# Kernel tuning notes

Measured on AMD Instinct MI355X. Metric: run time of the kernel, lower is better.

The kernel has to match this reference:

```python
import jax, jax.numpy as jnp
import numpy as np

EMB = 1024
NHEAD = 16
DILATIONS = (1, 4, 8, 16)
KSIZE = 7
ROT_DIM = 32  # RotaryEmbedding(dim=32): only first 32 channels of each head rotated


def neighbor_idx(T, k, d):
    # NATTEN-style 1D dilated neighborhood: window of k positions on the
    # dilation lattice (same residue class mod d), centered and clamped at borders.
    i = jnp.arange(T)
    r = i % d                      # residue class
    p = i // d                     # position within class
    Lr = (T - r + d - 1) // d      # class length
    s = jnp.clip(p - k // 2, 0, Lr - k)
    j = jnp.arange(k)
    return r[:, None] + (s[:, None] + j[None, :]) * d  # [T, k] int indices


def rope(x, rot_dim=ROT_DIM):
    # lucidrains RotaryEmbedding.rotate_queries_or_keys: interleaved pairs,
    # applied over seq dim (-2), only first rot_dim channels.
    T = x.shape[-2]
    inv = 1.0 / (10000.0 ** (jnp.arange(0, rot_dim, 2, dtype=jnp.float32) / rot_dim))
    freqs = jnp.arange(T, dtype=jnp.float32)[:, None] * inv[None, :]  # [T, rot_dim//2]
    freqs = jnp.repeat(freqs, 2, axis=-1)                             # [T, rot_dim]
    cos, sin = jnp.cos(freqs), jnp.sin(freqs)
    xr, xp = x[..., :rot_dim], x[..., rot_dim:]
    x1, x2 = xr[..., 0::2], xr[..., 1::2]
    rot = jnp.stack([-x2, x1], axis=-1).reshape(xr.shape)
    return jnp.concatenate([xr * cos + rot * sin, xp], axis=-1)


def setup_inputs() -> dict:
    key = jax.random.key(0)
    ks = jax.random.split(key, 5)
    B, T, C = 4, 8192, EMB
    s = 0.02
    return {
        "x": jax.random.normal(ks[0], (B, T, C), jnp.float32),
        "wq": jax.random.normal(ks[1], (C, C), jnp.float32) * s,
        "bq": jnp.zeros((C,), jnp.float32),
        "wk": jax.random.normal(ks[2], (C, C), jnp.float32) * s,
        "bk": jnp.zeros((C,), jnp.float32),
        "wv": jax.random.normal(ks[3], (C, C), jnp.float32) * s,
        "bv": jnp.zeros((C,), jnp.float32),
        "wp": jax.random.normal(ks[4], (C, C), jnp.float32) * s,
        "bp": jnp.zeros((C,), jnp.float32),
    }


def reference(x, wq, bq, wk, bk, wv, bv, wp, bp):
    B, T, C = x.shape
    hs = C // NHEAD

    def heads(w, b):  # torch Linear: x @ W^T + b, then [B, nh, T, hs]
        return (x @ w.T + b).reshape(B, T, NHEAD, hs).transpose(0, 2, 1, 3)

    q, k, v = heads(wq, bq), heads(wk, bk), heads(wv, bv)
    present = jnp.stack([k, v])  # pre-rotary kv cache, as in original

    q, k, v = rope(q), rope(k), rope(v)  # original also rotates v

    gsz = NHEAD // len(DILATIONS)
    outs = []
    for gi, d in enumerate(DILATIONS):
        sl = slice(gi * gsz, (gi + 1) * gsz)
        idx = neighbor_idx(T, KSIZE, d)           # [T, K]
        kk = k[:, sl][:, :, idx]                   # [B, g, T, K, hs]
        vv = v[:, sl][:, :, idx]                   # [B, g, T, K, hs]
        scores = jnp.einsum('bgtd,bgtkd->bgtk', q[:, sl], kk)  # no 1/sqrt(hs), as na1d_qk
        attn = jax.nn.softmax(scores, axis=-1)
        outs.append(jnp.einsum('bgtk,bgtkd->bgtd', attn, vv))
    y = jnp.concatenate(outs, axis=1)              # [B, nh, T, hs]
    y = y.transpose(0, 2, 1, 3).reshape(B, T, C)
    y = y @ wp.T + bp
    return (y, present)
```

## Files before the change

### kernel.cpp

```cpp
#include <hip/hip_runtime.h>

typedef unsigned short ushortT;
typedef unsigned int uint32;
typedef __attribute__((ext_vector_type(8))) short short8;
typedef __attribute__((ext_vector_type(4))) float f32x4;

__device__ __forceinline__ ushortT f2bf(float f) {
    uint32 u = __float_as_uint(f);
    uint32 r = (u + 0x7fffu + ((u >> 16) & 1u)) >> 16;
    return (ushortT)r;
}
__device__ __forceinline__ float bf2f(uint32 v) {
    return __uint_as_float(v << 16);
}

__device__ __forceinline__ void unpack8(uint4 v, float* f) {
    f[0] = bf2f(v.x & 0xffffu); f[1] = bf2f(v.x >> 16);
    f[2] = bf2f(v.y & 0xffffu); f[3] = bf2f(v.y >> 16);
    f[4] = bf2f(v.z & 0xffffu); f[5] = bf2f(v.z >> 16);
    f[6] = bf2f(v.w & 0xffffu); f[7] = bf2f(v.w >> 16);
}

typedef __attribute__((address_space(1))) const void gvoid;
typedef __attribute__((address_space(3))) void lvoid;
__device__ __forceinline__ void gld16(const ushortT* g, ushortT* l) {
    __builtin_amdgcn_global_load_lds((gvoid*)g, (lvoid*)l, 16, 0, 0);
}

__global__ __launch_bounds__(256) void f32_to_bf16_kernel(
    const float* __restrict__ src, ushortT* __restrict__ dst, int n4)
{
    int i = blockIdx.x * 256 + threadIdx.x;
    if (i < n4) {
        float4 v = reinterpret_cast<const float4*>(src)[i];
        ushort4 o;
        o.x = f2bf(v.x); o.y = f2bf(v.y); o.z = f2bf(v.z); o.w = f2bf(v.w);
        reinterpret_cast<ushort4*>(dst)[i] = o;
    }
}

__global__ __launch_bounds__(256) void wconv_kernel(
    const float* __restrict__ s0, const float* __restrict__ s1,
    const float* __restrict__ s2, const float* __restrict__ s3,
    ushortT* __restrict__ dst)
{
    int i = blockIdx.x * 256 + threadIdx.x;
    const int wsel = i >> 18;
    const int off  = i & 262143;
    const float* s = (wsel == 0) ? s0 : (wsel == 1 ? s1 : (wsel == 2 ? s2 : s3));
    float4 v = reinterpret_cast<const float4*>(s)[off];
    ushort4 o;
    o.x = f2bf(v.x); o.y = f2bf(v.y); o.z = f2bf(v.z); o.w = f2bf(v.w);
    reinterpret_cast<ushort4*>(dst)[i] = o;
}

__global__ __launch_bounds__(256) void pack_bias_kernel(
    const float* __restrict__ bq, const float* __restrict__ bk,
    const float* __restrict__ bv, float* __restrict__ out)
{
    int i = blockIdx.x * 256 + threadIdx.x;
    float v = (i < 1024) ? bq[i] : (i < 2048 ? bk[i - 1024] : bv[i - 2048]);
    out[i] = v;
}

__global__ __launch_bounds__(256) void rope_table_kernel(float2* __restrict__ tab)
{
    int idx = blockIdx.x * 256 + threadIdx.x;
    int t = idx >> 4;
    int i = idx & 15;
    float inv = powf(10000.0f, -(float)i / 16.0f);
    float ang = (float)t * inv;
    tab[idx] = make_float2(cosf(ang), sinf(ang));
}


__device__ __forceinline__ short8 ldsfrag(const ushortT* region, int row, int g) {
    int e = (row << 5) + (g << 3);
    e ^= ((row >> 1) & 3) << 3;
    return *reinterpret_cast<const short8*>(region + e);
}

#define MC_ ((size_t)33554432)

template<int MODE>
__global__ __launch_bounds__(256, 3) void gemm128_kernel(
    const ushortT* __restrict__ A,
    const ushortT* __restrict__ Wall,
    const float*   __restrict__ biasAll,
    const float2*  __restrict__ tab,
    ushortT*       __restrict__ CbAll,
    float*         __restrict__ CfAll,
    int M, int N, int K)
{
    __shared__ ushortT lds[16384];
    const int tid  = threadIdx.x;
    const int lane = tid & 63;
    const int wv   = tid >> 6;
    const int wm   = wv >> 1;
    const int wn   = wv & 1;
    const int g    = lane >> 4;
    const int rsel = lane & 15;

    const int bidAll = blockIdx.x;
    const int proj   = (MODE == 3) ? (bidAll >> 11) : 0;
    const int bid    = (MODE == 3) ? (bidAll & 2047) : bidAll;

    const ushortT* W    = Wall + (size_t)proj * 1024 * K;
    const float*   bias = biasAll + proj * 1024;

    const int xi  = bid & 7;
    const int j   = bid >> 3;
    const int tn  = j & 7;
    const int tm  = xi * 32 + (j >> 3);
    const int m0  = tm * 128, n0 = tn * 128;

    const int crow = tid >> 2;
    const int ccol = ((tid & 3) ^ ((tid >> 3) & 3)) * 8;
    const ushortT* gA0 = A + (size_t)(m0 + crow) * K + ccol;
    const ushortT* gA1 = gA0 + (size_t)64 * K;
    const ushortT* gB0 = W + (size_t)(n0 + crow) * K + ccol;
    const ushortT* gB1 = gB0 + (size_t)64 * K;

    const int dst0 = wv * 512;
    const int dst1 = 2048 + wv * 512;

    #define STAGE(buf, t) { \
        ushortT* base_ = lds + (buf) * 8192; \
        gld16(gA0 + (t) * 32, base_ + dst0); \
        gld16(gA1 + (t) * 32, base_ + dst1); \
        gld16(gB0 + (t) * 32, base_ + 4096 + dst0); \
        gld16(gB1 + (t) * 32, base_ + 4096 + dst1); \
    }

    f32x4 acc[4][4] = {};
    const int NT = K >> 5;
    int cur = 0;

    STAGE(0, 0);

    #pragma unroll 1
    for (int t = 0; t < NT; ++t) {
        __syncthreads();
        if (t + 1 < NT) STAGE(cur ^ 1, t + 1);

        const ushortT* ra = lds + cur * 8192;
        const ushortT* rb = ra + 4096;
        short8 Af[4], Bf[4];
        #pragma unroll
        for (int fm = 0; fm < 4; ++fm) Af[fm] = ldsfrag(ra, wm * 64 + fm * 16 + rsel, g);
        #pragma unroll
        for (int fn = 0; fn < 4; ++fn) Bf[fn] = ldsfrag(rb, wn * 64 + fn * 16 + rsel, g);
        #pragma unroll
        for (int fm = 0; fm < 4; ++fm)
            #pragma unroll
            for (int fn = 0; fn < 4; ++fn)
                acc[fm][fn] = __builtin_amdgcn_mfma_f32_16x16x32_bf16(Af[fm], Bf[fn], acc[fm][fn], 0, 0, 0);
        cur ^= 1;
    }
    #undef STAGE

    #pragma unroll
    for (int fn = 0; fn < 4; ++fn) {
        const int colb = n0 + wn * 64 + fn * 16 + rsel;
        const int d    = colb & 63;
        const float bv = bias[colb];
        #pragma unroll
        for (int fm = 0; fm < 4; ++fm) {
            const int rowbase = m0 + wm * 64 + fm * 16 + g * 4;
            #pragma unroll
            for (int e = 0; e < 4; ++e) {
                const int row = rowbase + e;
                const float val = acc[fm][fn][e] + bv;
                if (MODE == 2) {
                    CfAll[(size_t)row * N + colb] = val;
                } else {
                    if (proj != 0) {
                        const int b = row >> 13, t = row & 8191;
                        const int h = colb >> 6;
                        CfAll[(size_t)(proj - 1) * MC_ +
                              (((size_t)b * 16 + h) * 8192 + t) * 64 + d] = val;
                    }
                    const float pv = __shfl_xor(val, 1, 64);
                    float ov = val;
                    if (d < 32) {
                        const int t = row & 8191;
                        const float2 cs = tab[t * 16 + (d >> 1)];
                        ov = (d & 1) ? fmaf(val, cs.x,  pv * cs.y)
                                     : fmaf(val, cs.x, -pv * cs.y);
                    }
                    CbAll[(size_t)proj * MC_ + (size_t)row * 1024 + colb] = f2bf(ov);
                }
            }
        }
    }
}

__global__ __launch_bounds__(256) void natt_kernel(
    const ushortT* __restrict__ Q,
    const ushortT* __restrict__ Kl,
    const ushortT* __restrict__ Vl,
    ushortT*       __restrict__ O)
{
    const int T = 8192;
    const int tid  = threadIdx.x;
    const int lane = tid & 63;
    const int tloc = lane >> 3;
    const int c    = lane & 7;

    const int wq   = (blockIdx.x * 256 + tid) >> 6;
    const int qidx = wq * 8 + tloc;
    const int t = qidx & (T - 1);
    const int h = (qidx >> 13) & 15;
    const int b = qidx >> 17;

    const int shifts[4] = {0, 2, 3, 4};
    const int sh = shifts[h >> 2];
    const int dd = 1 << sh;

    const int r  = t & (dd - 1);
    const int p  = t >> sh;
    const int Lr = ((T - 1 - r) >> sh) + 1;
    int s = p - 3;
    const int smax = Lr - 7;
    s = s < 0 ? 0 : (s > smax ? smax : s);
    const int tbase = r + (s << sh);

    const size_t qoff = ((size_t)(b * T + t)) * 1024 + h * 64 + c * 8;
    float qf[8];
    unpack8(*reinterpret_cast<const uint4*>(Q + qoff), qf);

    const size_t cbase = ((size_t)b * T) * 1024 + h * 64 + c * 8;

    float sc[7];
    #pragma unroll
    for (int j = 0; j < 7; ++j) {
        const int tj = tbase + (j << sh);
        float kf[8];
        unpack8(*reinterpret_cast<const uint4*>(Kl + cbase + (size_t)tj * 1024), kf);
        float pp = 0.f;
        #pragma unroll
        for (int i = 0; i < 8; ++i) pp = fmaf(qf[i], kf[i], pp);
        pp += __shfl_xor(pp, 1, 64);
        pp += __shfl_xor(pp, 2, 64);
        pp += __shfl_xor(pp, 4, 64);
        sc[j] = pp;
    }

    float mx = sc[0];
    #pragma unroll
    for (int j = 1; j < 7; ++j) mx = fmaxf(mx, sc[j]);
    float den = 0.f;
    #pragma unroll
    for (int j = 0; j < 7; ++j) { sc[j] = __expf(sc[j] - mx); den += sc[j]; }
    const float inv = 1.0f / den;

    float out[8] = {};
    #pragma unroll
    for (int j = 0; j < 7; ++j) {
        const int tj = tbase + (j << sh);
        float vf[8];
        unpack8(*reinterpret_cast<const uint4*>(Vl + cbase + (size_t)tj * 1024), vf);
        #pragma unroll
        for (int i = 0; i < 8; ++i) out[i] = fmaf(sc[j], vf[i], out[i]);
    }

    short8 ov;
    #pragma unroll
    for (int i = 0; i < 8; ++i) ov[i] = (short)f2bf(out[i] * inv);
    *reinterpret_cast<short8*>(const_cast<ushortT*>(O + qoff)) = ov;
}

extern "C" void kernel_launch(void* const* d_in, const int* in_sizes, int n_in,
                              void* d_out, int out_size, void* d_ws, size_t ws_size,
                              hipStream_t stream)
{
    const float* x  = (const float*)d_in[0];
    const float* wq = (const float*)d_in[1];
    const float* bq = (const float*)d_in[2];
    const float* wk = (const float*)d_in[3];
    const float* bk = (const float*)d_in[4];
    const float* wv = (const float*)d_in[5];
    const float* bv = (const float*)d_in[6];
    const float* wp = (const float*)d_in[7];
    const float* bp = (const float*)d_in[8];

    const int B = 4, T = 8192, C = 1024;
    const int M = B * T;
    const size_t MC = (size_t)M * C;

    char* ws = (char*)d_ws;
    ushortT* xb    = (ushortT*)ws;
    ushortT* wallb = (ushortT*)(ws + (size_t)64 * 1024 * 1024);
    ushortT* wpb   = wallb + (size_t)3 * C * C;
    ushortT* qlin  = (ushortT*)(ws + (size_t)72 * 1024 * 1024);
    ushortT* klin  = qlin + MC;
    ushortT* vlin  = klin + MC;
    float2*  tab   = (float2*)(ws + (size_t)264 * 1024 * 1024);
    float*   bqkv  = (float*)(ws + (size_t)266 * 1024 * 1024);

    float* y     = (float*)d_out;
    float* presK = y + MC;

    rope_table_kernel<<<512, 256, 0, stream>>>(tab);
    pack_bias_kernel<<<12, 256, 0, stream>>>(bq, bk, bv, bqkv);

    f32_to_bf16_kernel<<<(int)(MC / 4 / 256), 256, 0, stream>>>(x, xb, (int)(MC / 4));
    wconv_kernel<<<4 * (C * C / 4) / 256, 256, 0, stream>>>(wq, wk, wv, wp, wallb);

    gemm128_kernel<3><<<6144, 256, 0, stream>>>(
        xb, wallb, bqkv, tab, qlin, presK, M, C, C);

    natt_kernel<<<(B * 16 * T) / 32, 256, 0, stream>>>(qlin, klin, vlin, xb);

    gemm128_kernel<2><<<2048, 256, 0, stream>>>(
        xb, wpb, bp, tab, nullptr, y, M, C, C);
}
```

Measured before the change: 587.3 us.

## Fuse Q/K/V projections into one GEMM sharing the A tile

The QKV projection kernel now computes all three projections in each block, using a 128x64 tile per projection. Each staged A tile therefore feeds three B tiles instead of being reloaded once per projection, which cuts A-side global and LDS traffic. The trade-off is a larger accumulator set (96 floats per lane) and more shared memory, so the launch bound drops to 2 blocks per CU and occupancy may fall. The output projection becomes its own specialised kernel with launch bound 4.

Result: slower. 716.1 us (+21.9%).

```diff
diff --git a/kernel.cpp b/kernel.cpp
--- a/kernel.cpp
+++ b/kernel.cpp
@@ -73,7 +73,6 @@
     tab[idx] = make_float2(cosf(ang), sinf(ang));
 }
 
-
 __device__ __forceinline__ short8 ldsfrag(const ushortT* region, int row, int g) {
     int e = (row << 5) + (g << 3);
     e ^= ((row >> 1) & 3) << 3;
@@ -82,17 +81,16 @@
 
 #define MC_ ((size_t)33554432)
 
-template<int MODE>
-__global__ __launch_bounds__(256, 3) void gemm128_kernel(
+__global__ __launch_bounds__(256, 2) void gemm_qkv_kernel(
     const ushortT* __restrict__ A,
     const ushortT* __restrict__ Wall,
     const float*   __restrict__ biasAll,
     const float2*  __restrict__ tab,
     ushortT*       __restrict__ CbAll,
     float*         __restrict__ CfAll,
-    int M, int N, int K)
-{
-    __shared__ ushortT lds[16384];
+    int M, int K)
+{
+    __shared__ ushortT lds[2 * 10240];
     const int tid  = threadIdx.x;
     const int lane = tid & 63;
     const int wv   = tid >> 6;
@@ -101,38 +99,35 @@
     const int g    = lane >> 4;
     const int rsel = lane & 15;
 
-    const int bidAll = blockIdx.x;
-    const int proj   = (MODE == 3) ? (bidAll >> 11) : 0;
-    const int bid    = (MODE == 3) ? (bidAll & 2047) : bidAll;
-
-    const ushortT* W    = Wall + (size_t)proj * 1024 * K;
-    const float*   bias = biasAll + proj * 1024;
-
+    const int bid = blockIdx.x;
     const int xi  = bid & 7;
     const int j   = bid >> 3;
-    const int tn  = j & 7;
-    const int tm  = xi * 32 + (j >> 3);
-    const int m0  = tm * 128, n0 = tn * 128;
+    const int tn  = j & 15;
+    const int tm  = xi * 32 + (j >> 4);
+    const int m0  = tm * 128, n0 = tn * 64;
 
     const int crow = tid >> 2;
     const int ccol = ((tid & 3) ^ ((tid >> 3) & 3)) * 8;
     const ushortT* gA0 = A + (size_t)(m0 + crow) * K + ccol;
     const ushortT* gA1 = gA0 + (size_t)64 * K;
-    const ushortT* gB0 = W + (size_t)(n0 + crow) * K + ccol;
-    const ushortT* gB1 = gB0 + (size_t)64 * K;
-
-    const int dst0 = wv * 512;
-    const int dst1 = 2048 + wv * 512;
+    const ushortT* gBq = Wall + (size_t)(n0 + crow) * K + ccol;
+    const ushortT* gBk = gBq + (size_t)1024 * K;
+    const ushortT* gBv = gBq + (size_t)2048 * K;
+
+    const int dA0 = wv * 512;
+    const int dA1 = 2048 + wv * 512;
+    const int dB  = wv * 512;
 
     #define STAGE(buf, t) { \
-        ushortT* base_ = lds + (buf) * 8192; \
-        gld16(gA0 + (t) * 32, base_ + dst0); \
-        gld16(gA1 + (t) * 32, base_ + dst1); \
-        gld16(gB0 + (t) * 32, base_ + 4096 + dst0); \
-        gld16(gB1 + (t) * 32, base_ + 4096 + dst1); \
-    }
-
-    f32x4 acc[4][4] = {};
+        ushortT* b_ = lds + (buf) * 10240; \
+        gld16(gA0 + (t) * 32, b_ + dA0); \
+        gld16(gA1 + (t) * 32, b_ + dA1); \
+        gld16(gBq + (t) * 32, b_ + 4096 + dB); \
+        gld16(gBk + (t) * 32, b_ + 6144 + dB); \
+        gld16(gBv + (t) * 32, b_ + 8192 + dB); \
+    }
+
+    f32x4 acc[3][4][2] = {};
     const int NT = K >> 5;
     int cur = 0;
 
@@ -143,41 +138,47 @@
         __syncthreads();
         if (t + 1 < NT) STAGE(cur ^ 1, t + 1);
 
-        const ushortT* ra = lds + cur * 8192;
-        const ushortT* rb = ra + 4096;
-        short8 Af[4], Bf[4];
-        #pragma unroll
-        for (int fm = 0; fm < 4; ++fm) Af[fm] = ldsfrag(ra, wm * 64 + fm * 16 + rsel, g);
-        #pragma unroll
-        for (int fn = 0; fn < 4; ++fn) Bf[fn] = ldsfrag(rb, wn * 64 + fn * 16 + rsel, g);
+        const ushortT* bb = lds + cur * 10240;
+        short8 Af[4], Bf[3][2];
         #pragma unroll
         for (int fm = 0; fm < 4; ++fm)
+            Af[fm] = ldsfrag(bb, wm * 64 + fm * 16 + rsel, g);
+        #pragma unroll
+        for (int p = 0; p < 3; ++p)
             #pragma unroll
-            for (int fn = 0; fn < 4; ++fn)
-                acc[fm][fn] = __builtin_amdgcn_mfma_f32_16x16x32_bf16(Af[fm], Bf[fn], acc[fm][fn], 0, 0, 0);
+            for (int fn = 0; fn < 2; ++fn)
+                Bf[p][fn] = ldsfrag(bb + 4096 + p * 2048, wn * 32 + fn * 16 + rsel, g);
+
+        #pragma unroll
+        for (int p = 0; p < 3; ++p)
+            #pragma unroll
+            for (int fm = 0; fm < 4; ++fm)
+                #pragma unroll
+                for (int fn = 0; fn < 2; ++fn)
+                    acc[p][fm][fn] = __builtin_amdgcn_mfma_f32_16x16x32_bf16(
+                        Af[fm], Bf[p][fn], acc[p][fm][fn], 0, 0, 0);
         cur ^= 1;
     }
     #undef STAGE
 
     #pragma unroll
-    for (int fn = 0; fn < 4; ++fn) {
-        const int colb = n0 + wn * 64 + fn * 16 + rsel;
-        const int d    = colb & 63;
-        const float bv = bias[colb];
-        #pragma unroll
-        for (int fm = 0; fm < 4; ++fm) {
-            const int rowbase = m0 + wm * 64 + fm * 16 + g * 4;
+    for (int p = 0; p < 3; ++p) {
+        #pragma unroll
+        for (int fn = 0; fn < 2; ++fn) {
+            const int colb = n0 + wn * 32 + fn * 16 + rsel;
+            const int d    = colb & 63;
+            const float bv = biasAll[p * 1024 + colb];
             #pragma unroll
-            for (int e = 0; e < 4; ++e) {
-                const int row = rowbase + e;
-                const float val = acc[fm][fn][e] + bv;
-                if (MODE == 2) {
-                    CfAll[(size_t)row * N + colb] = val;
-                } else {
-                    if (proj != 0) {
+            for (int fm = 0; fm < 4; ++fm) {
+                const int rowbase = m0 + wm * 64 + fm * 16 + g * 4;
+                #pragma unroll
+                for (int e = 0; e < 4; ++e) {
+                    const int row = rowbase + e;
+                    const float val = acc[p][fm][fn][e] + bv;
+                    if (p != 0) {
                         const int b = row >> 13, t = row & 8191;
                         const int h = colb >> 6;
-                        CfAll[(size_t)(proj - 1) * MC_ +
+                        CfAll[(size_t)(p - 1) * MC_ +
                               (((size_t)b * 16 + h) * 8192 + t) * 64 + d] = val;
                     }
                     const float pv = __shfl_xor(val, 1, 64);
@@ -188,8 +189,92 @@
                         ov = (d & 1) ? fmaf(val, cs.x,  pv * cs.y)
                                      : fmaf(val, cs.x, -pv * cs.y);
                     }
-                    CbAll[(size_t)proj * MC_ + (size_t)row * 1024 + colb] = f2bf(ov);
+                    CbAll[(size_t)p * MC_ + (size_t)row * 1024 + colb] = f2bf(ov);
                 }
+            }
+        }
+    }
+}
+
+__global__ __launch_bounds__(256, 4) void gemm_out_kernel(
+    const ushortT* __restrict__ A,
+    const ushortT* __restrict__ W,
+    const float*   __restrict__ bias,
+    float*         __restrict__ Cf,
+    int M, int N, int K)
+{
+    __shared__ ushortT lds[2 * 8192];
+    const int tid  = threadIdx.x;
+    const int lane = tid & 63;
+    const int wv   = tid >> 6;
+    const int wm   = wv >> 1;
+    const int wn   = wv & 1;
+    const int g    = lane >> 4;
+    const int rsel = lane & 15;
+
+    const int bid = blockIdx.x;
+    const int xi  = bid & 7;
+    const int j   = bid >> 3;
+    const int tn  = j & 7;
+    const int tm  = xi * 32 + (j >> 3);
+    const int m0  = tm * 128, n0 = tn * 128;
+
+    const int crow = tid >> 2;
+    const int ccol = ((tid & 3) ^ ((tid >> 3) & 3)) * 8;
+    const ushortT* gA0 = A + (size_t)(m0 + crow) * K + ccol;
+    const ushortT* gA1 = gA0 + (size_t)64 * K;
+    const ushortT* gB0 = W + (size_t)(n0 + crow) * K + ccol;
+    const ushortT* gB1 = gB0 + (size_t)64 * K;
+
+    const int dst0 = wv * 512;
+    const int dst1 = 2048 + wv * 512;
+
+    #define STAGE(buf, t) { \
+        ushortT* b_ = lds + (buf) * 8192; \
+        gld16(gA0 + (t) * 32, b_ + dst0); \
+        gld16(gA1 + (t) * 32, b_ + dst1); \
+        gld16(gB0 + (t) * 32, b_ + 4096 + dst0); \
+        gld16(gB1 + (t) * 32, b_ + 4096 + dst1); \
+    }
+
+    f32x4 acc[4][4] = {};
+    const int NT = K >> 5;
+    int cur = 0;
+
+    STAGE(0, 0);
+
+    #pragma unroll 1
+    for (int t = 0; t < NT; ++t) {
+        __syncthreads();
+        if (t + 1 < NT) STAGE(cur ^ 1, t + 1);
+
+        const ushortT* ra = lds + cur * 8192;
+        const ushortT* rb = ra + 4096;
+        short8 Af[4], Bf[4];
+        #pragma unroll
+        for (int fm = 0; fm < 4; ++fm) Af[fm] = ldsfrag(ra, wm * 64 + fm * 16 + rsel, g);
+        #pragma unroll
+        for (int fn = 0; fn < 4; ++fn) Bf[fn] = ldsfrag(rb, wn * 64 + fn * 16 + rsel, g);
+        #pragma unroll
+        for (int fm = 0; fm < 4; ++fm)
+            #pragma unroll
+            for (int fn = 0; fn < 4; ++fn)
+                acc[fm][fn] = __builtin_amdgcn_mfma_f32_16x16x32_bf16(Af[fm], Bf[fn], acc[fm][fn], 0, 0, 0);
+        cur ^= 1;
+    }
+    #undef STAGE
+
+    #pragma unroll
+    for (int fn = 0; fn < 4; ++fn) {
+        const int colb = n0 + wn * 64 + fn * 16 + rsel;
+        const float bv = bias[colb];
+        #pragma unroll
+        for (int fm = 0; fm < 4; ++fm) {
+            const int rowbase = m0 + wm * 64 + fm * 16 + g * 4;
+            #pragma unroll
+            for (int e = 0; e < 4; ++e) {
+                const int row = rowbase + e;
+                Cf[(size_t)row * N + colb] = acc[fm][fn][e] + bv;
             }
         }
     }
@@ -307,11 +392,11 @@
     f32_to_bf16_kernel<<<(int)(MC / 4 / 256), 256, 0, stream>>>(x, xb, (int)(MC / 4));
     wconv_kernel<<<4 * (C * C / 4) / 256, 256, 0, stream>>>(wq, wk, wv, wp, wallb);
 
-    gemm128_kernel<3><<<6144, 256, 0, stream>>>(
-        xb, wallb, bqkv, tab, qlin, presK, M, C, C);
+    gemm_qkv_kernel<<<4096, 256, 0, stream>>>(
+        xb, wallb, bqkv, tab, qlin, presK, M, C);
 
     natt_kernel<<<(B * 16 * T) / 32, 256, 0, stream>>>(qlin, klin, vlin, xb);
 
-    gemm128_kernel<2><<<2048, 256, 0, stream>>>(
-        xb, wpb, bp, tab, nullptr, y, M, C, C);
-}
+    gemm_out_kernel<<<2048, 256, 0, stream>>>(
+        xb, wpb, bp, y, M, C, C);
+}
```
